# Performance work log

Hardware: AMD Instinct MI355X
Metric: run time of the kernel (lower is better)

## Reference

```python
import jax, jax.numpy as jnp
import numpy as np

T = 8          # message-passing steps (hparams['T'])
D = 64         # link_state_dim
R = 128        # readout_units
E = 100000     # num edges (rows of link_state)
M = 400000     # num messages (len of states_first/second)
G = 1000       # num graphs in the batch


def _gru_cell(x, h, W, U, b):
    """Keras GRUCell with reset_after=True. x:[N,in], h:[N,units].
    W:[in,3u], U:[u,3u], b:[2,3u] (input bias, recurrent bias)."""
    mx = x @ W + b[0]
    mh = h @ U + b[1]
    xz, xr, xh = jnp.split(mx, 3, axis=-1)
    hz, hr, hh = jnp.split(mh, 3, axis=-1)
    z = jax.nn.sigmoid(xz + hz)
    r = jax.nn.sigmoid(xr + hr)
    cand = jnp.tanh(xh + r * hh)
    return z * h + (1.0 - z) * cand


def setup_inputs() -> dict:
    key = jax.random.key(0)
    ks = jax.random.split(key, 12)
    glorot = jax.nn.initializers.glorot_uniform()
    inp = {
        "link_state": jax.random.normal(ks[0], (E, D), jnp.float32),
        "states_first": jax.random.randint(ks[1], (M,), 0, E, jnp.int32),
        "states_second": jax.random.randint(ks[2], (M,), 0, E, jnp.int32),
        "states_graph_ids": jnp.sort(jax.random.randint(ks[3], (E,), 0, G, jnp.int32)),
        "num_edges": E,
        # Message MLP: Dense(D) with selu on concat [*, 2D]
        "W_msg": glorot(ks[4], (2 * D, D), jnp.float32),
        "b_msg": jnp.zeros((D,), jnp.float32),
        # Update GRUCell (units=D, input dim=D)
        "W_upd": glorot(ks[5], (D, 3 * D), jnp.float32),
        "U_upd": glorot(ks[6], (D, 3 * D), jnp.float32),
        "b_upd": jnp.zeros((2, 3 * D), jnp.float32),
        # Readout GRU (units=R, input dim=D)
        "W_ro": glorot(ks[7], (D, 3 * R), jnp.float32),
        "U_ro": glorot(ks[8], (R, 3 * R), jnp.float32),
        "b_ro": jnp.zeros((2, 3 * R), jnp.float32),
        # Final Dense(1)
        "W_out": glorot(ks[9], (R, 1), jnp.float32),
        "b_out": jnp.zeros((1,), jnp.float32),
    }
    return inp


def reference(link_state, states_first, states_second, states_graph_ids, num_edges,
              W_msg, b_msg, W_upd, U_upd, b_upd, W_ro, U_ro, b_ro, W_out, b_out):
    def mp_step(h, _):
        # gather sender/receiver states, concat -> message MLP (selu)
        edges_concat = jnp.concatenate([h[states_first], h[states_second]], axis=1)  # [M, 2D]
        msg = jax.nn.selu(edges_concat @ W_msg + b_msg)                              # [M, D]
        # scatter-add messages to receiver edges
        agg = jax.ops.segment_sum(msg, states_second, num_segments=num_edges)        # [E, D]
        h_new = _gru_cell(agg, h, W_upd, U_upd, b_upd)                               # [E, D]
        return h_new, h_new

    _, seq = jax.lax.scan(mp_step, link_state, None, length=T)  # seq: [T, E, D]

    # Readout GRU over the T-step state sequence per edge; return last hidden state
    def ro_step(h, x_t):
        h_new = _gru_cell(x_t, h, W_ro, U_ro, b_ro)
        return h_new, None

    h0 = jnp.zeros((link_state.shape[0], R), link_state.dtype)
    historial, _ = jax.lax.scan(ro_step, h0, seq)               # [E, R]

    # sorted segment_sum over graph ids, then Dense(1)
    per_graph = jax.ops.segment_sum(historial, states_graph_ids, num_segments=G,
                                    indices_are_sorted=True)    # [G, R]
    return per_graph @ W_out + b_out                             # [G, 1]
```

## Files before the change

kernel.cpp:

```cpp
#include <hip/hip_runtime.h>
#include <hip/hip_bf16.h>

#define D 64
#define R 128
#define NSTEPS 8
#define SELU_SCALE 1.0507009873554805f
#define SELU_ALPHA 1.6732632423543772f
#define PADH 72
#define PADF 68
#define PADR 136

typedef _Float16 half8 __attribute__((ext_vector_type(8)));
typedef float f32x4 __attribute__((ext_vector_type(4)));

__device__ __forceinline__ float fast_sig(float x) {
    return __fdividef(1.0f, 1.0f + __expf(-x));
}
__device__ __forceinline__ float fast_tanh(float x) {
    float xc = fminf(fmaxf(x, -15.0f), 15.0f);
    float e = __expf(2.0f * xc);
    return 1.0f - __fdividef(2.0f, e + 1.0f);
}

__global__ __launch_bounds__(256) void swizzle_all(
    const float* __restrict__ Wm, const float* __restrict__ Wu,
    const float* __restrict__ Uu, const float* __restrict__ Wr,
    const float* __restrict__ Ur,
    _Float16* __restrict__ wWm, _Float16* __restrict__ wWu,
    _Float16* __restrict__ wUu, _Float16* __restrict__ wWr,
    _Float16* __restrict__ wUr)
{
    const float* src; _Float16* dst; int K, N;
    switch (blockIdx.y) {
        case 0: src = Wm; dst = wWm; K = 128; N = 64;  break;
        case 1: src = Wu; dst = wWu; K = 64;  N = 192; break;
        case 2: src = Uu; dst = wUu; K = 64;  N = 192; break;
        case 3: src = Wr; dst = wWr; K = 64;  N = 384; break;
        default: src = Ur; dst = wUr; K = 128; N = 384; break;
    }
    int idx = blockIdx.x * 256 + threadIdx.x;
    int KT = K >> 5;
    int total = KT * (N >> 4) * 512;
    if (idx >= total) return;
    int j = idx & 7;
    int lane = (idx >> 3) & 63;
    int kt = (idx >> 9) % KT;
    int nt = idx / (512 * KT);
    int k = 32 * kt + 8 * (lane >> 4) + j;
    int n = 16 * nt + (lane & 15);
    dst[idx] = (_Float16)src[(size_t)k * N + n];
}

__global__ __launch_bounds__(256) void h16_init(const float* __restrict__ src,
                                                _Float16* __restrict__ dst, int n) {
    int i = blockIdx.x * 256 + threadIdx.x;
    if (i < n) dst[i] = (_Float16)src[i];
}

__global__ __launch_bounds__(192) void bias_pack(const float* __restrict__ bu,
                                                 const float* __restrict__ brr,
                                                 float4* __restrict__ biasU,
                                                 float4* __restrict__ biasR) {
    int c = threadIdx.x;
    if (c < 64) {
        biasU[c] = make_float4(bu[c] + bu[192 + c], bu[64 + c] + bu[256 + c],
                               bu[128 + c], bu[320 + c]);
    } else {
        int cr = c - 64;
        biasR[cr] = make_float4(brr[cr] + brr[384 + cr], brr[128 + cr] + brr[512 + cr],
                                brr[256 + cr], brr[640 + cr]);
    }
}

__global__ __launch_bounds__(256) void hist_kernel(const int* __restrict__ second,
                                                   int* __restrict__ cnt, int M) {
    int m = blockIdx.x * 256 + threadIdx.x;
    if (m < M) atomicAdd(&cnt[second[m]], 1);
}

__global__ __launch_bounds__(256) void scan_bsum(const int* __restrict__ cnt,
                                                 int* __restrict__ bsum, int E) {
    int i = blockIdx.x * 256 + threadIdx.x;
    int tid = threadIdx.x;
    int v = (i < E) ? cnt[i] : 0;
    __shared__ int s[256];
    s[tid] = v;
    __syncthreads();
    #pragma unroll
    for (int d = 1; d < 256; d <<= 1) {
        int t = (tid >= d) ? s[tid - d] : 0;
        __syncthreads();
        s[tid] += t;
        __syncthreads();
    }
    if (tid == 255) bsum[blockIdx.x] = s[255];
}

__global__ __launch_bounds__(1024) void scan_part(int* __restrict__ bsum, int NB) {
    int tid = threadIdx.x;
    __shared__ int s[1024];
    int v = (tid < NB) ? bsum[tid] : 0;
    s[tid] = v;
    __syncthreads();
    #pragma unroll
    for (int d = 1; d < 1024; d <<= 1) {
        int t = (tid >= d) ? s[tid - d] : 0;
        __syncthreads();
        s[tid] += t;
        __syncthreads();
    }
    if (tid < NB) bsum[tid] = s[tid] - v;
}

__global__ __launch_bounds__(256) void scan_final(const int* __restrict__ cnt,
                                                  const int* __restrict__ bsum,
                                                  int* __restrict__ off, int E) {
    int i = blockIdx.x * 256 + threadIdx.x;
    int tid = threadIdx.x;
    int v = (i < E) ? cnt[i] : 0;
    __shared__ int s[256];
    s[tid] = v;
    __syncthreads();
    #pragma unroll
    for (int d = 1; d < 256; d <<= 1) {
        int t = (tid >= d) ? s[tid - d] : 0;
        __syncthreads();
        s[tid] += t;
        __syncthreads();
    }
    if (i < E) off[i] = bsum[blockIdx.x] + s[tid] - v;
}

__global__ __launch_bounds__(256) void scatter_kernel(const int* __restrict__ second,
                                                      const int* __restrict__ off,
                                                      int* __restrict__ cur,
                                                      int* __restrict__ perm, int M) {
    int m = blockIdx.x * 256 + threadIdx.x;
    if (m < M) {
        int s = second[m];
        int p = atomicAdd(&cur[s], 1);
        perm[off[s] + p] = m;
    }
}

__global__ __launch_bounds__(256) void bucket_sort(const int* __restrict__ off,
                                                   int* __restrict__ perm,
                                                   int E, int M) {
    int e = blockIdx.x * 256 + threadIdx.x;
    if (e >= E) return;
    int a = off[e];
    int b = (e == E - 1) ? M : off[e + 1];
    for (int i = a + 1; i < b; ++i) {
        int key = perm[i];
        int j = i - 1;
        while (j >= a && perm[j] > key) {
            perm[j + 1] = perm[j];
            --j;
        }
        perm[j + 1] = key;
    }
}

__global__ __launch_bounds__(256) void fs_pack(const int* __restrict__ first,
                                               const int* __restrict__ second,
                                               const int* __restrict__ perm,
                                               int2* __restrict__ fs, int M) {
    int m = blockIdx.x * 256 + threadIdx.x;
    if (m < M) {
        int pm = perm[m];
        fs[m] = make_int2(first[pm], second[pm]);
    }
}

__global__ __launch_bounds__(256) void msg_upd(
    const _Float16* __restrict__ hin,
    _Float16* __restrict__ hout,
    const int2* __restrict__ fs,
    const int* __restrict__ off,
    const half8* __restrict__ wBm,
    const float* __restrict__ bm,
    const half8* __restrict__ wWu,
    const half8* __restrict__ wUu,
    const float4* __restrict__ biasU,
    int E, int M)
{
    __shared__ _Float16 stage_s[4][16 * PADH];
    __shared__ float aggF_s[4][16 * PADF];
    __shared__ int skeys[4][16];

    const int wid = threadIdx.x >> 6;
    const int lane = threadIdx.x & 63;
    const int hi = lane >> 4;
    const int l15 = lane & 15;
    const int e0 = (blockIdx.x * 4 + wid) * 16;

    _Float16* stageH = stage_s[wid];
    float* aggF = aggF_s[wid];
    int* skey = skeys[wid];

    #pragma unroll
    for (int m = 0; m < 16; ++m)
        aggF[m * PADF + lane] = 0.0f;

    half8 Bm[4][4];
    #pragma unroll
    for (int nt = 0; nt < 4; ++nt)
        #pragma unroll
        for (int kt = 0; kt < 4; ++kt)
            Bm[nt][kt] = wBm[(nt * 4 + kt) * 64 + lane];

    if (e0 >= E) return;

    {
        int b = min(e0 + 16, E);
        int mstart = off[e0];
        int mend = (b == E) ? M : off[b];
        int nch = (mend > mstart) ? ((mend - mstart + 15) >> 4) : 0;

        int2 pcur = make_int2(0, 0);
        if (nch > 0) pcur = fs[min(mstart + l15, mend - 1)];

        #pragma unroll 1
        for (int ch = 0; ch < nch; ++ch) {
            int2 pnext = pcur;
            if (ch + 1 < nch)
                pnext = fs[min(mstart + (ch + 1) * 16 + l15, mend - 1)];

            const half8* fr = reinterpret_cast<const half8*>(hin + (size_t)pcur.x * D);
            const half8* sr = reinterpret_cast<const half8*>(hin + (size_t)pcur.y * D);
            half8 A[4];
            A[0] = fr[hi];
            A[1] = fr[4 + hi];
            A[2] = sr[hi];
            A[3] = sr[4 + hi];

            f32x4 acc[4];
            #pragma unroll
            for (int nt = 0; nt < 4; ++nt) acc[nt] = (f32x4){0.f, 0.f, 0.f, 0.f};
            #pragma unroll
            for (int nt = 0; nt < 4; ++nt)
                #pragma unroll
                for (int kt = 0; kt < 4; ++kt)
                    acc[nt] = __builtin_amdgcn_mfma_f32_16x16x32_f16(A[kt], Bm[nt][kt], acc[nt], 0, 0, 0);

            #pragma unroll
            for (int nt = 0; nt < 4; ++nt) {
                int n = nt * 16 + l15;
                float bias = bm[n];
                #pragma unroll
                for (int r = 0; r < 4; ++r) {
                    float v = acc[nt][r] + bias;
                    v = (v > 0.0f) ? (SELU_SCALE * v)
                                   : (SELU_SCALE * SELU_ALPHA) * (__expf(v) - 1.0f);
                    stageH[(hi * 4 + r) * PADH + n] = (_Float16)v;
                }
            }
            {
                int mrow = mstart + ch * 16 + l15;
                if (lane < 16) skey[lane] = (mrow < mend) ? (pcur.y - e0) : -1;
            }

            float run = 0.0f;
            int kprev = skey[0];
            #pragma unroll
            for (int m = 0; m < 16; ++m) {
                int km = skey[m];
                if (km != kprev) {
                    if (kprev >= 0) aggF[kprev * PADF + lane] += run;
                    run = 0.0f;
                    kprev = km;
                }
                run += (float)stageH[m * PADH + lane];
            }
            if (kprev >= 0) aggF[kprev * PADF + lane] += run;

            pcur = pnext;
        }
    }

    const int ec = min(e0 + l15, E - 1);

    half8 AX[2], AHu[2];
    #pragma unroll
    for (int kt = 0; kt < 2; ++kt) {
        const float* s = aggF + l15 * PADF + 32 * kt + 8 * hi;
        half8 ax;
        #pragma unroll
        for (int j = 0; j < 8; ++j) ax[j] = (_Float16)s[j];
        AX[kt] = ax;
        AHu[kt] = reinterpret_cast<const half8*>(hin + (size_t)ec * D)[4 * kt + hi];
    }

    #pragma unroll 1
    for (int i = 0; i < 4; ++i) {
        half8 WBz[2], WBr[2], WBc[2], UBz[2], UBr[2], UBc[2];
        #pragma unroll
        for (int kt = 0; kt < 2; ++kt) {
            WBz[kt] = wWu[((0 + i) * 2 + kt) * 64 + lane];
            WBr[kt] = wWu[((4 + i) * 2 + kt) * 64 + lane];
            WBc[kt] = wWu[((8 + i) * 2 + kt) * 64 + lane];
            UBz[kt] = wUu[((0 + i) * 2 + kt) * 64 + lane];
            UBr[kt] = wUu[((4 + i) * 2 + kt) * 64 + lane];
            UBc[kt] = wUu[((8 + i) * 2 + kt) * 64 + lane];
        }
        int n = 16 * i + l15;
        float4 bU = biasU[n];

        f32x4 az  = (f32x4){0.f, 0.f, 0.f, 0.f};
        f32x4 ar_ = (f32x4){0.f, 0.f, 0.f, 0.f};
        f32x4 acx = (f32x4){0.f, 0.f, 0.f, 0.f};
        f32x4 ach = (f32x4){0.f, 0.f, 0.f, 0.f};
        #pragma unroll
        for (int kt = 0; kt < 2; ++kt) {
            az  = __builtin_amdgcn_mfma_f32_16x16x32_f16(AX[kt], WBz[kt], az, 0, 0, 0);
            az  = __builtin_amdgcn_mfma_f32_16x16x32_f16(AHu[kt], UBz[kt], az, 0, 0, 0);
            ar_ = __builtin_amdgcn_mfma_f32_16x16x32_f16(AX[kt], WBr[kt], ar_, 0, 0, 0);
            ar_ = __builtin_amdgcn_mfma_f32_16x16x32_f16(AHu[kt], UBr[kt], ar_, 0, 0, 0);
            acx = __builtin_amdgcn_mfma_f32_16x16x32_f16(AX[kt], WBc[kt], acx, 0, 0, 0);
            ach = __builtin_amdgcn_mfma_f32_16x16x32_f16(AHu[kt], UBc[kt], ach, 0, 0, 0);
        }
        #pragma unroll
        for (int r = 0; r < 4; ++r) {
            int e = e0 + hi * 4 + r;
            int ecl = min(e, E - 1);
            float z = fast_sig(az[r] + bU.x);
            float rr = fast_sig(ar_[r] + bU.y);
            float c = fast_tanh(acx[r] + bU.z + rr * (ach[r] + bU.w));
            float hp = (float)hin[(size_t)ecl * D + n];
            float hn = z * hp + (1.0f - z) * c;
            if (e < E) hout[(size_t)e * D + n] = (_Float16)hn;
        }
    }
}

__global__ __launch_bounds__(512, 2) void ro_all(
    const _Float16* __restrict__ hseq1,
    const int* __restrict__ gid,
    const float* __restrict__ Wout,
    const half8* __restrict__ wWr,
    const half8* __restrict__ wUr,
    const float4* __restrict__ biasR,
    float* __restrict__ out,
    int E, int edelems)
{
    __shared__ _Float16 rot2[2][16 * PADR];
    __shared__ float partials[8][16];

    const int w = threadIdx.x >> 6;
    const int lane = threadIdx.x & 63;
    const int hi = lane >> 4;
    const int l15 = lane & 15;
    const int e0 = blockIdx.x * 16;
    const int ec = min(e0 + l15, E - 1);

    half8 WBz[2], WBr[2], WBx[2], UBz[4], UBr[4], UBh[4];
    #pragma unroll
    for (int kt = 0; kt < 2; ++kt) {
        WBz[kt] = wWr[((0 + w) * 2 + kt) * 64 + lane];
        WBr[kt] = wWr[((8 + w) * 2 + kt) * 64 + lane];
        WBx[kt] = wWr[((16 + w) * 2 + kt) * 64 + lane];
    }
    #pragma unroll
    for (int kt = 0; kt < 4; ++kt) {
        UBz[kt] = wUr[((0 + w) * 4 + kt) * 64 + lane];
        UBr[kt] = wUr[((8 + w) * 4 + kt) * 64 + lane];
        UBh[kt] = wUr[((16 + w) * 4 + kt) * 64 + lane];
    }
    const int c = w * 16 + l15;
    const float4 bR = biasR[c];

    half8 hp = {};

    half8 AXt[2];
    #pragma unroll
    for (int kt = 0; kt < 2; ++kt)
        AXt[kt] = reinterpret_cast<const half8*>(hseq1 + (size_t)ec * D)[4 * kt + hi];

    #pragma unroll 1
    for (int t = 0; t < NSTEPS; ++t) {
        f32x4 az  = (f32x4){0.f, 0.f, 0.f, 0.f};
        f32x4 ar_ = (f32x4){0.f, 0.f, 0.f, 0.f};
        f32x4 acx = (f32x4){0.f, 0.f, 0.f, 0.f};
        f32x4 ach = (f32x4){0.f, 0.f, 0.f, 0.f};
        #pragma unroll
        for (int kt = 0; kt < 2; ++kt) {
            az  = __builtin_amdgcn_mfma_f32_16x16x32_f16(AXt[kt], WBz[kt], az, 0, 0, 0);
            ar_ = __builtin_amdgcn_mfma_f32_16x16x32_f16(AXt[kt], WBr[kt], ar_, 0, 0, 0);
            acx = __builtin_amdgcn_mfma_f32_16x16x32_f16(AXt[kt], WBx[kt], acx, 0, 0, 0);
        }

        if (t + 1 < NSTEPS) {
            const _Float16* hn = hseq1 + (size_t)(t + 1) * edelems;
            #pragma unroll
            for (int kt = 0; kt < 2; ++kt)
                AXt[kt] = reinterpret_cast<const half8*>(hn + (size_t)ec * D)[4 * kt + hi];
        }

        if (t > 0) {
            _Float16* rotile = rot2[t & 1];
            #pragma unroll
            for (int r = 0; r < 4; ++r)
                rotile[(hi * 4 + r) * PADR + w * 16 + l15] = hp[r];
            __syncthreads();

            half8 AHro[4];
            #pragma unroll
            for (int kt = 0; kt < 4; ++kt)
                AHro[kt] = *reinterpret_cast<const half8*>(&rotile[l15 * PADR + 32 * kt + 8 * hi]);

            #pragma unroll
            for (int kt = 0; kt < 4; ++kt) {
                az  = __builtin_amdgcn_mfma_f32_16x16x32_f16(AHro[kt], UBz[kt], az, 0, 0, 0);
                ar_ = __builtin_amdgcn_mfma_f32_16x16x32_f16(AHro[kt], UBr[kt], ar_, 0, 0, 0);
                ach = __builtin_amdgcn_mfma_f32_16x16x32_f16(AHro[kt], UBh[kt], ach, 0, 0, 0);
            }
        }

        #pragma unroll
        for (int r = 0; r < 4; ++r) {
            float z = fast_sig(az[r] + bR.x);
            float rr = fast_sig(ar_[r] + bR.y);
            float cc = fast_tanh(acx[r] + bR.z + rr * (ach[r] + bR.w));
            float hpf = (float)hp[r];
            hp[r] = (_Float16)(z * hpf + (1.0f - z) * cc);
        }
    }

    const float wv = Wout[c];
    float part[4];
    #pragma unroll
    for (int r = 0; r < 4; ++r) part[r] = (float)hp[r] * wv;
    #pragma unroll
    for (int d = 1; d < 16; d <<= 1) {
        #pragma unroll
        for (int r = 0; r < 4; ++r)
            part[r] += __shfl_xor(part[r], d);
    }
    if (l15 == 0) {
        #pragma unroll
        for (int r = 0; r < 4; ++r)
            partials[w][hi * 4 + r] = part[r];
    }
    __syncthreads();
    if (w == 0 && lane < 16) {
        float s = 0.0f;
        #pragma unroll
        for (int ww = 0; ww < 8; ++ww) s += partials[ww][lane];
        int e = e0 + lane;
        if (e < E) unsafeAtomicAdd(out + gid[e], s);
    }
}

__global__ void out_init_kernel(float* __restrict__ out, const float* __restrict__ b_out, int G) {
    int g = blockIdx.x * blockDim.x + threadIdx.x;
    if (g < G) out[g] = b_out[0];
}

extern "C" void kernel_launch(void* const* d_in, const int* in_sizes, int n_in,
                              void* d_out, int out_size, void* d_ws, size_t ws_size,
                              hipStream_t stream) {
    const float* link_state = (const float*)d_in[0];
    const int*   first      = (const int*)d_in[1];
    const int*   second     = (const int*)d_in[2];
    const int*   gids       = (const int*)d_in[3];
    const float* Wm         = (const float*)d_in[5];
    const float* bm         = (const float*)d_in[6];
    const float* Wu         = (const float*)d_in[7];
    const float* Uu         = (const float*)d_in[8];
    const float* bu         = (const float*)d_in[9];
    const float* Wr         = (const float*)d_in[10];
    const float* Ur         = (const float*)d_in[11];
    const float* brb        = (const float*)d_in[12];
    const float* Wout       = (const float*)d_in[13];
    const float* bout       = (const float*)d_in[14];

    const int E = in_sizes[0] / D;
    const int M = in_sizes[1];
    const int G = out_size;

    char* p = (char*)d_ws;
    auto carve = [&](size_t bytes) {
        void* r = (void*)p;
        p += (bytes + 255) & ~(size_t)255;
        return r;
    };
    const size_t edelems = (size_t)E * D;
    _Float16*  hseq  = (_Float16*)carve(edelems * 2 * (NSTEPS + 1));
    int*       perm  = (int*)carve((size_t)M * 4);
    int2*      fs    = (int2*)carve((size_t)M * 8);
    int*       cnt   = (int*)carve((size_t)E * 4);
    int*       cur   = (int*)carve((size_t)E * 4);
    int*       off   = (int*)carve((size_t)(E + 1) * 4);
    int*       bsum  = (int*)carve(4096 * 4);
    _Float16*  wWm   = (_Float16*)carve(8192 * 2);
    _Float16*  wWu   = (_Float16*)carve(12288 * 2);
    _Float16*  wUu   = (_Float16*)carve(12288 * 2);
    _Float16*  wWr   = (_Float16*)carve(24576 * 2);
    _Float16*  wUr   = (_Float16*)carve(49152 * 2);
    float4*    biasU = (float4*)carve(64 * 16);
    float4*    biasR = (float4*)carve(128 * 16);

    hipMemsetAsync(cnt, 0, (size_t)E * 4, stream);
    hipMemsetAsync(cur, 0, (size_t)E * 4, stream);

    h16_init<<<(E * D + 255) / 256, 256, 0, stream>>>(link_state, hseq, E * D);
    swizzle_all<<<dim3(192, 5), 256, 0, stream>>>(Wm, Wu, Uu, Wr, Ur,
                                                  wWm, wWu, wUu, wWr, wUr);
    bias_pack<<<1, 192, 0, stream>>>(bu, brb, biasU, biasR);

    const int NB = (E + 255) / 256;
    hist_kernel<<<(M + 255) / 256, 256, 0, stream>>>(second, cnt, M);
    scan_bsum<<<NB, 256, 0, stream>>>(cnt, bsum, E);
    scan_part<<<1, 1024, 0, stream>>>(bsum, NB);
    scan_final<<<NB, 256, 0, stream>>>(cnt, bsum, off, E);
    scatter_kernel<<<(M + 255) / 256, 256, 0, stream>>>(second, off, cur, perm, M);
    bucket_sort<<<NB, 256, 0, stream>>>(off, perm, E, M);
    fs_pack<<<(M + 255) / 256, 256, 0, stream>>>(first, second, perm, fs, M);

    const int e_blocks = (E + 63) / 64;

    for (int t = 0; t < NSTEPS; ++t) {
        msg_upd<<<e_blocks, 256, 0, stream>>>(hseq + (size_t)t * edelems,
                                              hseq + (size_t)(t + 1) * edelems,
                                              fs, off,
                                              (const half8*)wWm, bm,
                                              (const half8*)wWu, (const half8*)wUu, biasU,
                                              E, M);
    }

    out_init_kernel<<<(G + 255) / 256, 256, 0, stream>>>((float*)d_out, bout, G);
    const int ro_blocks = (E + 15) / 16;
    ro_all<<<ro_blocks, 512, 0, stream>>>(hseq + edelems, gids, Wout,
                                          (const half8*)wWr, (const half8*)wUr, biasR,
                                          (float*)d_out, E, (int)edelems);
}
```

Before: 752.9 us.

## Replace LDS run-length segment sum with one-hot MFMA aggregation

Message rows are no longer staged to shared memory and scanned serially to accumulate per-edge sums. A 16x16 one-hot selection matrix is built from the receiver keys and multiplied by the SELU messages with MFMA, keeping aggregates in registers. This removes the float shared-memory aggregation buffer and the serial 16-step loop per chunk. Message values are rounded to fp16 before summation, the same as the old staging path.

```diff
diff --git a/kernel.cpp b/kernel.cpp
--- a/kernel.cpp
+++ b/kernel.cpp
@@ -7,10 +7,10 @@
 #define SELU_SCALE 1.0507009873554805f
 #define SELU_ALPHA 1.6732632423543772f
 #define PADH 72
-#define PADF 68
 #define PADR 136
 
 typedef _Float16 half8 __attribute__((ext_vector_type(8)));
+typedef _Float16 half4 __attribute__((ext_vector_type(4)));
 typedef float f32x4 __attribute__((ext_vector_type(4)));
 
 __device__ __forceinline__ float fast_sig(float x) {
@@ -185,7 +185,6 @@
     int E, int M)
 {
     __shared__ _Float16 stage_s[4][16 * PADH];
-    __shared__ float aggF_s[4][16 * PADF];
     __shared__ int skeys[4][16];
 
     const int wid = threadIdx.x >> 6;
@@ -195,12 +194,7 @@
     const int e0 = (blockIdx.x * 4 + wid) * 16;
 
     _Float16* stageH = stage_s[wid];
-    float* aggF = aggF_s[wid];
     int* skey = skeys[wid];
-
-    #pragma unroll
-    for (int m = 0; m < 16; ++m)
-        aggF[m * PADF + lane] = 0.0f;
 
     half8 Bm[4][4];
     #pragma unroll
@@ -210,6 +204,10 @@
             Bm[nt][kt] = wBm[(nt * 4 + kt) * 64 + lane];
 
     if (e0 >= E) return;
+
+    f32x4 agg[4];
+    #pragma unroll
+    for (int nt = 0; nt < 4; ++nt) agg[nt] = (f32x4){0.f, 0.f, 0.f, 0.f};
 
     {
         int b = min(e0 + 16, E);
@@ -243,51 +241,46 @@
                 for (int kt = 0; kt < 4; ++kt)
                     acc[nt] = __builtin_amdgcn_mfma_f32_16x16x32_f16(A[kt], Bm[nt][kt], acc[nt], 0, 0, 0);
 
+            {
+                int mrow = mstart + ch * 16 + l15;
+                if (lane < 16) skey[lane] = (mrow < mend) ? (pcur.y - e0) : -1;
+            }
+            half4 Sf;
+            #pragma unroll
+            for (int j = 0; j < 4; ++j)
+                Sf[j] = (skey[4 * hi + j] == l15) ? (_Float16)1.0f : (_Float16)0.0f;
+
             #pragma unroll
             for (int nt = 0; nt < 4; ++nt) {
                 int n = nt * 16 + l15;
                 float bias = bm[n];
+                half4 Bf;
                 #pragma unroll
                 for (int r = 0; r < 4; ++r) {
                     float v = acc[nt][r] + bias;
                     v = (v > 0.0f) ? (SELU_SCALE * v)
                                    : (SELU_SCALE * SELU_ALPHA) * (__expf(v) - 1.0f);
-                    stageH[(hi * 4 + r) * PADH + n] = (_Float16)v;
+                    Bf[r] = (_Float16)v;
                 }
+                agg[nt] = __builtin_amdgcn_mfma_f32_16x16x16f16(Sf, Bf, agg[nt], 0, 0, 0);
             }
-            {
-                int mrow = mstart + ch * 16 + l15;
-                if (lane < 16) skey[lane] = (mrow < mend) ? (pcur.y - e0) : -1;
-            }
-
-            float run = 0.0f;
-            int kprev = skey[0];
-            #pragma unroll
-            for (int m = 0; m < 16; ++m) {
-                int km = skey[m];
-                if (km != kprev) {
-                    if (kprev >= 0) aggF[kprev * PADF + lane] += run;
-                    run = 0.0f;
-                    kprev = km;
-                }
-                run += (float)stageH[m * PADH + lane];
-            }
-            if (kprev >= 0) aggF[kprev * PADF + lane] += run;
 
             pcur = pnext;
         }
     }
 
+    #pragma unroll
+    for (int nt = 0; nt < 4; ++nt)
+        #pragma unroll
+        for (int r = 0; r < 4; ++r)
+            stageH[(hi * 4 + r) * PADH + nt * 16 + l15] = (_Float16)agg[nt][r];
+
     const int ec = min(e0 + l15, E - 1);
 
     half8 AX[2], AHu[2];
     #pragma unroll
     for (int kt = 0; kt < 2; ++kt) {
-        const float* s = aggF + l15 * PADF + 32 * kt + 8 * hi;
-        half8 ax;
-        #pragma unroll
-        for (int j = 0; j < 8; ++j) ax[j] = (_Float16)s[j];
-        AX[kt] = ax;
+        AX[kt] = *reinterpret_cast<const half8*>(&stageH[l15 * PADH + 32 * kt + 8 * hi]);
         AHu[kt] = reinterpret_cast<const half8*>(hin + (size_t)ec * D)[4 * kt + hi];
     }
 
```

After: 803.4 us. +6.7%, slower.
